# Kernel tuning notes

Measured on AMD Instinct MI355X. Metric: run time of the kernel, lower is better.

The kernel has to match this reference:

```python
import jax, jax.numpy as jnp
import numpy as np
import math

N_TOTAL = 262144
C = 128
B = 512
LMAX = 512  # max segment length (static for jit)


def setup_inputs() -> dict:
    key = jax.random.key(0)
    ks = jax.random.split(key, 8)
    Q_feature = jax.random.normal(ks[0], (N_TOTAL, C), dtype=jnp.float32)
    K_feature = jax.random.normal(ks[1], (N_TOTAL, C), dtype=jnp.float32)
    # cumulative offsets: equal segments of length LMAX (general code handles ragged)
    offset = (jnp.arange(1, B + 1, dtype=jnp.int64) * (N_TOTAL // B))
    s = 1.0 / math.sqrt(C)
    Wq = jax.random.normal(ks[2], (C, C), dtype=jnp.float32) * s
    Wk = jax.random.normal(ks[3], (C, C), dtype=jnp.float32) * s
    Wv = jax.random.normal(ks[4], (C, C), dtype=jnp.float32) * s
    bq = jnp.zeros((C,), dtype=jnp.float32)
    bk = jnp.zeros((C,), dtype=jnp.float32)
    bv = jnp.zeros((C,), dtype=jnp.float32)
    return {"Q_feature": Q_feature, "K_feature": K_feature,
            "Wq": Wq, "bq": bq, "Wk": Wk, "bk": bk, "Wv": Wv, "bv": bv,
            "offset": offset}


def reference(Q_feature, K_feature, Wq, bq, Wk, bk, Wv, bv, offset):
    N, Cdim = Q_feature.shape
    Q = Q_feature @ Wq.T + bq
    K = K_feature @ Wk.T + bk
    V = K_feature @ Wv.T + bv

    starts = jnp.concatenate([jnp.zeros((1,), offset.dtype), offset[:-1]])
    lengths = offset - starts                         # (B,)
    pos = jnp.arange(LMAX)                            # (LMAX,)
    idx = jnp.clip(starts[:, None] + pos[None, :], 0, N - 1)  # (B, LMAX)
    mask = pos[None, :] < lengths[:, None]            # (B, LMAX) valid tokens

    Qp = Q[idx]                                       # (B, LMAX, C)
    Kp = K[idx]
    Vp = V[idx]

    scale = 1.0 / math.sqrt(Cdim)
    scores = jnp.einsum('blc,bmc->blm', Qp, Kp) * scale     # (B, LMAX, LMAX)
    scores = jnp.where(mask[:, None, :], scores, jnp.float32(-1e30))
    attn = jax.nn.softmax(scores, axis=-1)
    outp = jnp.einsum('blm,bmc->blc', attn, Vp)             # (B, LMAX, C)
    outp = outp * mask[:, :, None]                          # zero padded rows

    # scatter padded segments back to flat (N, C); idx is an exact partition on valid rows
    out = jnp.zeros((N, Cdim), dtype=outp.dtype).at[idx].add(outp)
    return out
```

## Files before the change

kernel.cpp:

```cpp
#include <hip/hip_runtime.h>
#include <hip/hip_bf16.h>

#define CDIM 128
#define LMAXC 512
#define QBLK 128
#define KVBLK 64

#define QSCALE (0.08838834764831845f * 1.4426950408889634f)

typedef __attribute__((ext_vector_type(8))) short bf16x8;
typedef __attribute__((ext_vector_type(4))) short bf16x4;
typedef __attribute__((ext_vector_type(4))) float f32x4;

__device__ inline short f2bf(float f) {
    union { float f; unsigned u; } v; v.f = f;
    unsigned r = v.u + 0x7FFFu + ((v.u >> 16) & 1u);
    return (short)(r >> 16);
}

__device__ inline bf16x8 cvt8v(float4 a, float4 b) {
    bf16x8 o;
    o[0] = f2bf(a.x); o[1] = f2bf(a.y); o[2] = f2bf(a.z); o[3] = f2bf(a.w);
    o[4] = f2bf(b.x); o[5] = f2bf(b.y); o[6] = f2bf(b.z); o[7] = f2bf(b.w);
    return o;
}

__device__ inline unsigned pk2(float lo, float hi) {
    unsigned r;
    asm("v_cvt_pk_bf16_f32 %0, %1, %2" : "=v"(r) : "v"(lo), "v"(hi));
    return r;
}

__device__ inline void gload16(const void* g, void* l) {
    __builtin_amdgcn_global_load_lds(
        (const __attribute__((address_space(1))) unsigned*)g,
        (__attribute__((address_space(3))) unsigned*)l, 16, 0, 0);
}

__device__ inline void blk_barrier() {
    __builtin_amdgcn_sched_barrier(0);
    __builtin_amdgcn_s_barrier();
    __builtin_amdgcn_sched_barrier(0);
}

__device__ inline int pch(int q) { return ((q + (q >> 3)) & 7) << 4; }

__global__ void wcvt_kernel(const float* __restrict__ Wq,
                            const float* __restrict__ Wk,
                            const float* __restrict__ Wv,
                            short* __restrict__ Wbf)
{
    int t = blockIdx.x * 256 + threadIdx.x;
    int m = t / 2048;
    int e = (t % 2048) * 8;
    const float* W = (m == 0) ? Wq : (m == 1) ? Wk : Wv;
    float sc = (m == 0) ? QSCALE : 1.0f;
    float4 a = *reinterpret_cast<const float4*>(W + e);
    float4 b = *reinterpret_cast<const float4*>(W + e + 4);
    a.x *= sc; a.y *= sc; a.z *= sc; a.w *= sc;
    b.x *= sc; b.y *= sc; b.z *= sc; b.w *= sc;
    *reinterpret_cast<bf16x8*>(Wbf + m * 16384 + e) = cvt8v(a, b);
}

__device__ inline void tile_qk(const char* __restrict__ wlds,
                               const bf16x8 xfr[2][4],
                               const float* __restrict__ bias, float bsc,
                               short* __restrict__ outp, int rowb,
                               int lrow, int lhalf)
{
#pragma unroll
    for (int cf = 0; cf < 8; ++cf) {
        const int key = cf * 16 + lrow;
        bf16x8 wfr[4];
#pragma unroll
        for (int ks = 0; ks < 4; ++ks) {
            int wb = (key * 256 + (ks * 32 + lhalf * 8) * 2) ^ ((key & 7) << 4);
            wfr[ks] = *reinterpret_cast<const bf16x8*>(wlds + wb);
        }
        float4 bv4 = *reinterpret_cast<const float4*>(bias + cf * 16 + lhalf * 4);
#pragma unroll
        for (int xt = 0; xt < 2; ++xt) {
            f32x4 acc = {0.f, 0.f, 0.f, 0.f};
#pragma unroll
            for (int ks = 0; ks < 4; ++ks)
                acc = __builtin_amdgcn_mfma_f32_16x16x32_bf16(wfr[ks], xfr[xt][ks], acc, 0, 0, 0);
            bf16x4 pk;
            pk[0] = f2bf(acc[0] + bv4.x * bsc);
            pk[1] = f2bf(acc[1] + bv4.y * bsc);
            pk[2] = f2bf(acc[2] + bv4.z * bsc);
            pk[3] = f2bf(acc[3] + bv4.w * bsc);
            *reinterpret_cast<bf16x4*>(
                outp + (size_t)(rowb + xt * 16 + lrow) * CDIM
                     + cf * 16 + lhalf * 4) = pk;
        }
    }
}

__device__ inline void tile_v(const char* __restrict__ wlds,
                              const bf16x8 xfr[2][4],
                              const float* __restrict__ bv,
                              short* __restrict__ Vt, int rowb, int N,
                              int lrow, int lhalf)
{
#pragma unroll
    for (int cf = 0; cf < 8; ++cf) {
        const int d = cf * 16 + lrow;
        bf16x8 wfr[4];
#pragma unroll
        for (int ks = 0; ks < 4; ++ks) {
            int wb = (d * 256 + (ks * 32 + lhalf * 8) * 2) ^ ((d & 7) << 4);
            wfr[ks] = *reinterpret_cast<const bf16x8*>(wlds + wb);
        }
        f32x4 acc0 = {0.f, 0.f, 0.f, 0.f};
        f32x4 acc1 = {0.f, 0.f, 0.f, 0.f};
#pragma unroll
        for (int ks = 0; ks < 4; ++ks) {
            acc0 = __builtin_amdgcn_mfma_f32_16x16x32_bf16(xfr[0][ks], wfr[ks], acc0, 0, 0, 0);
            acc1 = __builtin_amdgcn_mfma_f32_16x16x32_bf16(xfr[1][ks], wfr[ks], acc1, 0, 0, 0);
        }
        float bcol = bv[d];
        bf16x4 p0, p1;
#pragma unroll
        for (int r = 0; r < 4; ++r) {
            p0[r] = f2bf(acc0[r] + bcol);
            p1[r] = f2bf(acc1[r] + bcol);
        }
        short* vrow = Vt + (size_t)d * N + rowb + lhalf * 4;
        *reinterpret_cast<bf16x4*>(vrow)      = p0;
        *reinterpret_cast<bf16x4*>(vrow + 16) = p1;
    }
}

__global__ __launch_bounds__(512) void proj_kernel(
    const float* __restrict__ Qf, const float* __restrict__ Kf,
    const short* __restrict__ Wbf,
    const float* __restrict__ bq, const float* __restrict__ bk,
    const float* __restrict__ bv,
    short* __restrict__ Qp, short* __restrict__ Kp, short* __restrict__ Vt,
    int N)
{
    __shared__ __align__(16) char wlds[32768];

    const int tid   = threadIdx.x;
    const int lane  = tid & 63;
    const int wv    = tid >> 6;
    const int lrow  = lane & 15;
    const int lhalf = lane >> 4;
    const int row0  = blockIdx.x * 256;
    const bool isQ  = (blockIdx.y == 0);
    const float* X  = isQ ? Qf : Kf;
    const int rowb  = row0 + wv * 32;

    const short* Wg = isQ ? Wbf : Wbf + 16384;
#pragma unroll
    for (int j = 0; j < 4; ++j) {
        int beta = j * 8192 + tid * 16;
        int r  = beta >> 8;
        int gs = ((beta >> 4) & 15) ^ (r & 7);
        gload16(Wg + r * 128 + gs * 8, wlds + beta);
    }

    bf16x8 xfr[2][4];
#pragma unroll
    for (int xt = 0; xt < 2; ++xt) {
        const float* xr = X + (size_t)(rowb + xt * 16 + lrow) * CDIM + lhalf * 8;
#pragma unroll
        for (int ks = 0; ks < 4; ++ks) {
            const float4* s = reinterpret_cast<const float4*>(xr + ks * 32);
            xfr[xt][ks] = cvt8v(s[0], s[1]);
        }
    }
    __syncthreads();

    if (isQ) {
        tile_qk(wlds, xfr, bq, QSCALE, Qp, rowb, lrow, lhalf);
    } else {
        tile_qk(wlds, xfr, bk, 1.0f, Kp, rowb, lrow, lhalf);
        __syncthreads();
#pragma unroll
        for (int j = 0; j < 4; ++j) {
            int beta = j * 8192 + tid * 16;
            int r  = beta >> 8;
            int gs = ((beta >> 4) & 15) ^ (r & 7);
            gload16(Wbf + 32768 + r * 128 + gs * 8, wlds + beta);
        }
        __syncthreads();
        tile_v(wlds, xfr, bv, Vt, rowb, N, lrow, lhalf);
    }
}

__global__ __launch_bounds__(256) void attn_kernel(
    const short* __restrict__ Qp, const short* __restrict__ Kp,
    const short* __restrict__ VtG, const int* __restrict__ offset,
    float* __restrict__ out, int Ntot)
{
    __shared__ __align__(16) char smem[81920];
    char* lds_p = smem + 65536;

    const int nq = LMAXC / QBLK;
    int flat = blockIdx.x, total = gridDim.x;
    int seg, qb;
    if ((total & (8 * nq - 1)) == 0) {
        int per = total >> 3;
        int xcd = flat & 7;
        int wi  = flat >> 3;
        int sl  = wi / nq;
        qb  = wi - sl * nq;
        seg = xcd * (per / nq) + sl;
    } else { seg = flat / nq; qb = flat - seg * nq; }

    const int start = (seg == 0) ? 0 : offset[seg - 1];
    int len = offset[seg] - start;
    if (len > LMAXC) len = LMAXC;
    const int q0 = qb * QBLK;
    if (q0 >= len) return;

    const int tid   = threadIdx.x;
    const int lane  = tid & 63;
    const int wv    = tid >> 6;
    const int lrow  = lane & 15;
    const int lhalf = lane >> 4;
    const int ntiles = (len + KVBLK - 1) / KVBLK;
    const int lm1 = len - 1;

    auto stage = [&](int kv0, int bb) {
        char* kb = smem + bb * 32768;
        char* vb = kb + 16384;
#pragma unroll
        for (int j = 0; j < 4; ++j) {
            int beta = j * 4096 + wv * 1024 + (lane << 4);
            int r  = beta >> 8;
            int gs = ((beta >> 4) & 15) ^ (r & 7);
            int rg = kv0 + r; if (rg > lm1) rg = lm1;
            gload16(Kp + (((size_t)(start + rg)) << 7) + (gs << 3),
                    kb + j * 4096 + wv * 1024);
            int d   = beta >> 7;
            int gs2 = ((beta >> 4) & 7) ^ (d & 7);
            long gk = (long)start + kv0 + (gs2 << 3);
            if (gk + 8 > Ntot) gk = Ntot - 8;
            gload16(VtG + (size_t)d * Ntot + gk,
                    vb + j * 4096 + wv * 1024);
        }
    };

    stage(0, 0);

    bf16x8 aq[2][4];
#pragma unroll
    for (int qt = 0; qt < 2; ++qt) {
        int qr = q0 + wv * 32 + qt * 16 + lrow;
        if (qr > lm1) qr = lm1;
        const short* qrow = Qp + (size_t)(start + qr) * CDIM;
#pragma unroll
        for (int ks = 0; ks < 4; ++ks)
            aq[qt][ks] = *reinterpret_cast<const bf16x8*>(qrow + ks * 32 + lhalf * 8);
    }

    f32x4 acc_o[2][8];
    float lsum[2] = {0.f, 0.f};
#pragma unroll
    for (int qt = 0; qt < 2; ++qt)
#pragma unroll
        for (int df = 0; df < 8; ++df) acc_o[qt][df] = (f32x4){0.f, 0.f, 0.f, 0.f};

    const int wbase = wv * 4096;

    for (int t = 0; t < ntiles; ++t) {
        const int kv0 = t * KVBLK;
        const int bb  = t & 1;
        if (t + 1 < ntiles) {
            stage(kv0 + KVBLK, bb ^ 1);
            asm volatile("s_waitcnt vmcnt(8)" ::: "memory");
        } else {
            asm volatile("s_waitcnt vmcnt(0)" ::: "memory");
        }
        blk_barrier();

        char* lds_k  = smem + bb * 32768;
        char* lds_vt = lds_k + 16384;
        const bool tail = (kv0 + KVBLK > len);

        f32x4 s0[4], s1[4];
        __builtin_amdgcn_s_setprio(1);
#pragma unroll
        for (int kf = 0; kf < 4; ++kf) {
            s0[kf] = (f32x4){0.f, 0.f, 0.f, 0.f};
            s1[kf] = (f32x4){0.f, 0.f, 0.f, 0.f};
            int key = kf * 16 + lrow;
#pragma unroll
            for (int ks = 0; ks < 4; ++ks) {
                int kbo = (key * 256 + (ks * 32 + lhalf * 8) * 2) ^ ((key & 7) << 4);
                bf16x8 kfr = *reinterpret_cast<const bf16x8*>(lds_k + kbo);
                s0[kf] = __builtin_amdgcn_mfma_f32_16x16x32_bf16(kfr, aq[0][ks], s0[kf], 0, 0, 0);
                s1[kf] = __builtin_amdgcn_mfma_f32_16x16x32_bf16(kfr, aq[1][ks], s1[kf], 0, 0, 0);
            }
        }
        __builtin_amdgcn_s_setprio(0);

        const int keyb0 = kv0 + lhalf * 4;
#pragma unroll
        for (int qt = 0; qt < 2; ++qt) {
            const int qlocal = qt * 16 + lrow;
            const int rowoff = wbase + qlocal * 128;
            const int swz = pch(qlocal);
#pragma unroll
            for (int kf = 0; kf < 4; ++kf) {
                f32x4 sv = qt ? s1[kf] : s0[kf];
                float p[4];
#pragma unroll
                for (int r = 0; r < 4; ++r) {
                    float pv = exp2f(sv[r]);
                    if (tail && (keyb0 + kf * 16 + r >= len)) pv = 0.f;
                    p[r] = pv;
                    lsum[qt] += pv;
                }
                unsigned long long w =
                    (unsigned long long)pk2(p[0], p[1]) |
                    ((unsigned long long)pk2(p[2], p[3]) << 32);
                *reinterpret_cast<unsigned long long*>(
                    lds_p + rowoff + ((kf * 32 + lhalf * 8) ^ swz)) = w;
            }
        }

        __builtin_amdgcn_s_setprio(1);
#pragma unroll
        for (int ks2 = 0; ks2 < 2; ++ks2) {
            bf16x8 ap0 = *reinterpret_cast<const bf16x8*>(
                lds_p + wbase + lrow * 128 + ((ks2 * 64 + lhalf * 16) ^ pch(lrow)));
            bf16x8 ap1 = *reinterpret_cast<const bf16x8*>(
                lds_p + wbase + (16 + lrow) * 128 + ((ks2 * 64 + lhalf * 16) ^ pch(16 + lrow)));
            int k0 = ks2 * 32 + lhalf * 8;
#pragma unroll
            for (int df = 0; df < 8; ++df) {
                int d = df * 16 + lrow;
                int vb2 = (d * 128 + k0 * 2) ^ ((d & 7) << 4);
                bf16x8 bvf = *reinterpret_cast<const bf16x8*>(lds_vt + vb2);
                acc_o[0][df] = __builtin_amdgcn_mfma_f32_16x16x32_bf16(ap0, bvf, acc_o[0][df], 0, 0, 0);
                acc_o[1][df] = __builtin_amdgcn_mfma_f32_16x16x32_bf16(ap1, bvf, acc_o[1][df], 0, 0, 0);
            }
        }
        __builtin_amdgcn_s_setprio(0);

        blk_barrier();
    }

#pragma unroll
    for (int qt = 0; qt < 2; ++qt) {
        float l = lsum[qt];
        l += __shfl_xor(l, 16);
        l += __shfl_xor(l, 32);
        float rinv[4];
#pragma unroll
        for (int r = 0; r < 4; ++r)
            rinv[r] = 1.0f / __shfl(l, lhalf * 4 + r);
#pragma unroll
        for (int df = 0; df < 8; ++df)
#pragma unroll
            for (int r = 0; r < 4; ++r) {
                int qg = q0 + wv * 32 + qt * 16 + lhalf * 4 + r;
                if (qg < len)
                    out[(size_t)(start + qg) * CDIM + df * 16 + lrow]
                        = acc_o[qt][df][r] * rinv[r];
            }
    }
}

extern "C" void kernel_launch(void* const* d_in, const int* in_sizes, int n_in,
                              void* d_out, int out_size, void* d_ws, size_t ws_size,
                              hipStream_t stream) {
    const float* Qf = (const float*)d_in[0];
    const float* Kf = (const float*)d_in[1];
    const float* Wq = (const float*)d_in[2];
    const float* bq = (const float*)d_in[3];
    const float* Wk = (const float*)d_in[4];
    const float* bk = (const float*)d_in[5];
    const float* Wv = (const float*)d_in[6];
    const float* bv_ = (const float*)d_in[7];
    const int* offset = (const int*)d_in[8];

    const int N = in_sizes[0] / CDIM;
    const int B = in_sizes[8];

    short* Qp = (short*)d_ws;
    short* Kp = Qp + (size_t)N * CDIM;
    short* Vt = Kp + (size_t)N * CDIM;
    float* out = (float*)d_out;

    size_t base_need = (size_t)3 * N * CDIM * 2;
    short* Wbf = (ws_size >= base_need + 3 * 16384 * 2)
               ? (Vt + (size_t)N * CDIM) : (short*)d_out;

    wcvt_kernel<<<24, 256, 0, stream>>>(Wq, Wk, Wv, Wbf);

    dim3 pgrid(N / 256, 2);
    proj_kernel<<<pgrid, 512, 0, stream>>>(Qf, Kf, Wbf, bq, bk, bv_,
                                           Qp, Kp, Vt, N);

    attn_kernel<<<dim3(B * (LMAXC / QBLK)), 256, 0, stream>>>(
        Qp, Kp, Vt, offset, out, N);
}
```

Measured before the change: 249.5 us.

## Fuse Q projection into attention kernel, drop Q workspace round-trip

Removes the Q half of the projection kernel and instead computes each block's 128 Q rows inside the attention kernel from fp32 inputs, using MFMA with Wq read from global memory, staging the result through swizzled LDS to reshape it into A-operand fragments. This avoids writing and re-reading a bf16 Q buffer of N x C and cuts the projection grid in half. The cost is extra prologue latency in each attention block (fp32 Q loads, Wq fetches, an LDS transpose and a barrier) before the KV loop starts. The workspace layout is also reordered so the bf16 weights always sit at the front.

```diff
diff --git a/kernel.cpp b/kernel.cpp
--- a/kernel.cpp
+++ b/kernel.cpp
@@ -131,13 +131,10 @@
     }
 }
 
-__global__ __launch_bounds__(512) void proj_kernel(
-    const float* __restrict__ Qf, const float* __restrict__ Kf,
-    const short* __restrict__ Wbf,
-    const float* __restrict__ bq, const float* __restrict__ bk,
-    const float* __restrict__ bv,
-    short* __restrict__ Qp, short* __restrict__ Kp, short* __restrict__ Vt,
-    int N)
+__global__ __launch_bounds__(512) void projkv_kernel(
+    const float* __restrict__ Kf, const short* __restrict__ Wbf,
+    const float* __restrict__ bk, const float* __restrict__ bv,
+    short* __restrict__ Kp, short* __restrict__ Vt, int N)
 {
     __shared__ __align__(16) char wlds[32768];
 
@@ -146,24 +143,20 @@
     const int wv    = tid >> 6;
     const int lrow  = lane & 15;
     const int lhalf = lane >> 4;
-    const int row0  = blockIdx.x * 256;
-    const bool isQ  = (blockIdx.y == 0);
-    const float* X  = isQ ? Qf : Kf;
-    const int rowb  = row0 + wv * 32;
-
-    const short* Wg = isQ ? Wbf : Wbf + 16384;
+    const int rowb  = blockIdx.x * 256 + wv * 32;
+
 #pragma unroll
     for (int j = 0; j < 4; ++j) {
         int beta = j * 8192 + tid * 16;
         int r  = beta >> 8;
         int gs = ((beta >> 4) & 15) ^ (r & 7);
-        gload16(Wg + r * 128 + gs * 8, wlds + beta);
+        gload16(Wbf + 16384 + r * 128 + gs * 8, wlds + beta);
     }
 
     bf16x8 xfr[2][4];
 #pragma unroll
     for (int xt = 0; xt < 2; ++xt) {
-        const float* xr = X + (size_t)(rowb + xt * 16 + lrow) * CDIM + lhalf * 8;
+        const float* xr = Kf + (size_t)(rowb + xt * 16 + lrow) * CDIM + lhalf * 8;
 #pragma unroll
         for (int ks = 0; ks < 4; ++ks) {
             const float4* s = reinterpret_cast<const float4*>(xr + ks * 32);
@@ -172,27 +165,24 @@
     }
     __syncthreads();
 
-    if (isQ) {
-        tile_qk(wlds, xfr, bq, QSCALE, Qp, rowb, lrow, lhalf);
-    } else {
-        tile_qk(wlds, xfr, bk, 1.0f, Kp, rowb, lrow, lhalf);
-        __syncthreads();
-#pragma unroll
-        for (int j = 0; j < 4; ++j) {
-            int beta = j * 8192 + tid * 16;
-            int r  = beta >> 8;
-            int gs = ((beta >> 4) & 15) ^ (r & 7);
-            gload16(Wbf + 32768 + r * 128 + gs * 8, wlds + beta);
-        }
-        __syncthreads();
-        tile_v(wlds, xfr, bv, Vt, rowb, N, lrow, lhalf);
-    }
+    tile_qk(wlds, xfr, bk, 1.0f, Kp, rowb, lrow, lhalf);
+    __syncthreads();
+#pragma unroll
+    for (int j = 0; j < 4; ++j) {
+        int beta = j * 8192 + tid * 16;
+        int r  = beta >> 8;
+        int gs = ((beta >> 4) & 15) ^ (r & 7);
+        gload16(Wbf + 32768 + r * 128 + gs * 8, wlds + beta);
+    }
+    __syncthreads();
+    tile_v(wlds, xfr, bv, Vt, rowb, N, lrow, lhalf);
 }
 
 __global__ __launch_bounds__(256) void attn_kernel(
-    const short* __restrict__ Qp, const short* __restrict__ Kp,
-    const short* __restrict__ VtG, const int* __restrict__ offset,
-    float* __restrict__ out, int Ntot)
+    const float* __restrict__ Qf, const short* __restrict__ Wbf,
+    const float* __restrict__ bq,
+    const short* __restrict__ Kp, const short* __restrict__ VtG,
+    const int* __restrict__ offset, float* __restrict__ out, int Ntot)
 {
     __shared__ __align__(16) char smem[81920];
     char* lds_p = smem + 65536;
@@ -222,6 +212,59 @@
     const int lhalf = lane >> 4;
     const int ntiles = (len + KVBLK - 1) / KVBLK;
     const int lm1 = len - 1;
+
+    bf16x8 aq[2][4];
+    {
+        char* qstage = smem + 32768 + wv * 8192;
+
+        bf16x8 xq[2][4];
+#pragma unroll
+        for (int qt = 0; qt < 2; ++qt) {
+            int qr = q0 + wv * 32 + qt * 16 + lrow;
+            if (qr > lm1) qr = lm1;
+            const float* xr = Qf + (size_t)(start + qr) * CDIM + lhalf * 8;
+#pragma unroll
+            for (int ks = 0; ks < 4; ++ks) {
+                const float4* s = reinterpret_cast<const float4*>(xr + ks * 32);
+                xq[qt][ks] = cvt8v(s[0], s[1]);
+            }
+        }
+#pragma unroll
+        for (int cf = 0; cf < 8; ++cf) {
+            const int key = cf * 16 + lrow;
+            bf16x8 wfr[4];
+#pragma unroll
+            for (int ks = 0; ks < 4; ++ks)
+                wfr[ks] = *reinterpret_cast<const bf16x8*>(
+                    Wbf + key * CDIM + ks * 32 + lhalf * 8);
+            float4 bq4 = *reinterpret_cast<const float4*>(bq + cf * 16 + lhalf * 4);
+#pragma unroll
+            for (int qt = 0; qt < 2; ++qt) {
+                f32x4 acc = {0.f, 0.f, 0.f, 0.f};
+#pragma unroll
+                for (int ks = 0; ks < 4; ++ks)
+                    acc = __builtin_amdgcn_mfma_f32_16x16x32_bf16(wfr[ks], xq[qt][ks], acc, 0, 0, 0);
+                bf16x4 pk;
+                pk[0] = f2bf(acc[0] + bq4.x * QSCALE);
+                pk[1] = f2bf(acc[1] + bq4.y * QSCALE);
+                pk[2] = f2bf(acc[2] + bq4.z * QSCALE);
+                pk[3] = f2bf(acc[3] + bq4.w * QSCALE);
+                int ql = qt * 16 + lrow;
+                *reinterpret_cast<bf16x4*>(
+                    qstage + ql * 256 + ((cf * 32 + lhalf * 8) ^ pch(ql))) = pk;
+            }
+        }
+        asm volatile("s_waitcnt lgkmcnt(0)" ::: "memory");
+#pragma unroll
+        for (int qt = 0; qt < 2; ++qt) {
+            int ql = qt * 16 + lrow;
+#pragma unroll
+            for (int ks = 0; ks < 4; ++ks)
+                aq[qt][ks] = *reinterpret_cast<const bf16x8*>(
+                    qstage + ql * 256 + ((ks * 64 + lhalf * 16) ^ pch(ql)));
+        }
+    }
+    __syncthreads();
 
     auto stage = [&](int kv0, int bb) {
         char* kb = smem + bb * 32768;
@@ -245,17 +288,6 @@
 
     stage(0, 0);
 
-    bf16x8 aq[2][4];
-#pragma unroll
-    for (int qt = 0; qt < 2; ++qt) {
-        int qr = q0 + wv * 32 + qt * 16 + lrow;
-        if (qr > lm1) qr = lm1;
-        const short* qrow = Qp + (size_t)(start + qr) * CDIM;
-#pragma unroll
-        for (int ks = 0; ks < 4; ++ks)
-            aq[qt][ks] = *reinterpret_cast<const bf16x8*>(qrow + ks * 32 + lhalf * 8);
-    }
-
     f32x4 acc_o[2][8];
     float lsum[2] = {0.f, 0.f};
 #pragma unroll
@@ -381,21 +413,16 @@
     const int N = in_sizes[0] / CDIM;
     const int B = in_sizes[8];
 
-    short* Qp = (short*)d_ws;
-    short* Kp = Qp + (size_t)N * CDIM;
-    short* Vt = Kp + (size_t)N * CDIM;
+    short* Wbf = (short*)d_ws;
+    short* Kp  = Wbf + 3 * 16384;
+    short* Vt  = Kp + (size_t)N * CDIM;
     float* out = (float*)d_out;
 
-    size_t base_need = (size_t)3 * N * CDIM * 2;
-    short* Wbf = (ws_size >= base_need + 3 * 16384 * 2)
-               ? (Vt + (size_t)N * CDIM) : (short*)d_out;
-
     wcvt_kernel<<<24, 256, 0, stream>>>(Wq, Wk, Wv, Wbf);
 
-    dim3 pgrid(N / 256, 2);
-    proj_kernel<<<pgrid, 512, 0, stream>>>(Qf, Kf, Wbf, bq, bk, bv_,
-                                           Qp, Kp, Vt, N);
+    projkv_kernel<<<dim3(N / 256), 512, 0, stream>>>(Kf, Wbf, bk, bv_,
+                                                     Kp, Vt, N);
 
     attn_kernel<<<dim3(B * (LMAXC / QBLK)), 256, 0, stream>>>(
-        Qp, Kp, Vt, offset, out, N);
-}
+        Qf, Wbf, bq, Kp, Vt, offset, out, N);
+}
```

Result: faster. 234.6 us (-5.9%).
